# Performance work log

Hardware: AMD Instinct MI355X
Metric: run time of the kernel (lower is better)

Reference implementation:

```python
import jax, jax.numpy as jnp
import numpy as np

DIM, HEADS, DEPTH, SEQ, LOCAL_W = 1024, 16, 7, 2048, 64
HEAD_DIM = DIM // HEADS
SCALE = 1.0 / HEAD_DIM ** 0.5


def cantor_mask(S, depth, local_window):
    """Allowed (i,j): |i-j| within local window, OR |i-j| lies in the Cantor set
    under `depth` levels of ternary subdivision (no base-3 digit equals 1)."""
    idx = np.arange(S)
    d = np.abs(idx[:, None] - idx[None, :])
    x = d.copy()
    ok = np.ones_like(d, dtype=bool)
    for _ in range(depth):
        ok &= (x % 3) != 1
        x //= 3
    ok &= x == 0  # offset must be < 3**depth
    return jnp.asarray(ok | (d <= local_window))  # [S, S] bool


def setup_inputs() -> dict:
    key = jax.random.key(0)
    ks = jax.random.split(key, 8)
    B = 2
    s = 0.02
    return {
        "query": jax.random.normal(ks[0], (B, SEQ, DIM), jnp.float32),
        "key_value": jax.random.normal(ks[1], (B, SEQ, DIM), jnp.float32),
        "Wq": jax.random.normal(ks[2], (DIM, DIM), jnp.float32) * s,
        "bq": jnp.zeros((DIM,), jnp.float32),
        "Wkv": jax.random.normal(ks[3], (DIM, 2 * DIM), jnp.float32) * s,
        "bkv": jnp.zeros((2 * DIM,), jnp.float32),
        "Wo": jax.random.normal(ks[4], (DIM, DIM), jnp.float32) * s,
        "bo": jnp.zeros((DIM,), jnp.float32),
    }


def reference(query, key_value, Wq, bq, Wkv, bkv, Wo, bo):
    B, S, D = query.shape
    H, hd = HEADS, HEAD_DIM
    mask = cantor_mask(S, DEPTH, LOCAL_W)  # static [S, S] bool

    q = (query @ Wq + bq).reshape(B, S, H, hd).transpose(0, 2, 1, 3)  # [B,H,S,hd]
    kv = (key_value @ Wkv + bkv).reshape(B, S, 2, H, hd).transpose(2, 0, 3, 1, 4)
    k, v = kv[0], kv[1]  # [B,H,S,hd]

    scores = jnp.einsum("bhqd,bhkd->bhqk", q, k) * SCALE
    scores = jnp.where(mask, scores, jnp.finfo(scores.dtype).min)
    attn = jax.nn.softmax(scores, axis=-1)
    out = jnp.einsum("bhqk,bhkd->bhqd", attn, v)  # [B,H,S,hd]
    out = out.transpose(0, 2, 1, 3).reshape(B, S, D)
    return out @ Wo + bo
```

## Files before the change

### kernel.cpp

```cpp
#include <hip/hip_runtime.h>
#include <stdint.h>

typedef _Float16 half_t;
typedef __attribute__((ext_vector_type(8))) _Float16 half8;
typedef __attribute__((ext_vector_type(4))) _Float16 half4;
typedef __attribute__((ext_vector_type(4))) float floatx4;

#define SEQ 2048
#define NH 16
#define HD 64

#define MFMA16(a, b, c) __builtin_amdgcn_mfma_f32_16x16x16f16(a, b, c, 0, 0, 0)
#define MFMA32K(a, b, c) __builtin_amdgcn_mfma_f32_16x16x32_f16(a, b, c, 0, 0, 0)

#define QSCALE 0.1803368801111306f

__global__ __launch_bounds__(256) void prep(
    const float* __restrict__ query, const float* __restrict__ key_value,
    const float* __restrict__ Wq, const float* __restrict__ Wkv,
    const float* __restrict__ Wo, half_t* __restrict__ xq,
    half_t* __restrict__ xkv, half_t* __restrict__ wqT,
    half_t* __restrict__ wkvT, half_t* __restrict__ woT,
    uint8_t* __restrict__ tok, uint8_t* __restrict__ tok16,
    uint64_t* __restrict__ maskw) {
  int bx = blockIdx.x, tid = threadIdx.x;
  if (bx < 2048) {
    const float* s; half_t* d; int base;
    if (bx < 1024) { s = query; d = xq; base = bx * 4096; }
    else { s = key_value; d = xkv; base = (bx - 1024) * 4096; }
#pragma unroll
    for (int u = 0; u < 4; ++u) {
      int i = base + u * 1024 + tid * 4;
      floatx4 v = *(const floatx4*)(s + i);
      half4 h;
      h[0] = (half_t)v[0]; h[1] = (half_t)v[1];
      h[2] = (half_t)v[2]; h[3] = (half_t)v[3];
      *(half4*)(d + i) = h;
    }
    return;
  }
  if (bx < 4096) {
    __shared__ float tile[32][33];
    int tx = tid & 31, ty = tid >> 5;
    const int K = 1024;
#pragma unroll
    for (int u = 0; u < 2; ++u) {
      int t = (bx - 2048) * 2 + u;
      const float* W; half_t* Wt; int N, nt, kt;
      if (t < 1024) { W = Wq; Wt = wqT; N = 1024; nt = t & 31; kt = t >> 5; }
      else if (t < 3072) { int t2 = t - 1024; W = Wkv; Wt = wkvT; N = 2048; nt = t2 & 63; kt = t2 >> 6; }
      else { int t2 = t - 3072; W = Wo; Wt = woT; N = 1024; nt = t2 & 31; kt = t2 >> 5; }
      int n0 = nt * 32, k0 = kt * 32;
#pragma unroll
      for (int i = 0; i < 4; ++i)
        tile[ty + i * 8][tx] = W[(size_t)(k0 + ty + i * 8) * N + n0 + tx];
      __syncthreads();
#pragma unroll
      for (int i = 0; i < 4; ++i)
        Wt[(size_t)(n0 + ty + i * 8) * K + k0 + tx] = (half_t)tile[tx][ty + i * 8];
      __syncthreads();
    }
    return;
  }
  __shared__ uint8_t slut[2048];
  int ib = bx - 4096;
  for (int d = tid; d < 2048; d += 256) {
    int x = d;
    bool ok = true;
    for (int it = 0; it < 7; ++it) { ok &= ((x % 3) != 1); x /= 3; }
    ok &= (x == 0);
    slut[d] = (ok || d <= 64) ? 1 : 0;
  }
  __syncthreads();
  if (ib == 0) {
    if (tid < 64) {
      int delta = tid - 32;
      int lo = delta * 64 - 63, hi = delta * 64 + 63;
      uint8_t any = 0;
      for (int x = lo; x <= hi; ++x) {
        int a = x < 0 ? -x : x;
        if (a < 2048) any |= slut[a];
      }
      tok[tid] = any;
    }
    {
      int d16 = tid - 128;
      int ctr = d16 * 16;
      uint8_t any = 0;
      for (int x = ctr - 15; x <= ctr + 15; ++x) {
        int a = x < 0 ? -x : x;
        if (a < 2048) any |= slut[a];
      }
      tok16[tid] = any;
    }
  }
  int g = ib * 256 + tid;
  int tt = g - 2048;
  uint64_t w = 0;
  for (int jj = 0; jj < 64; ++jj) {
    int d = tt - jj; d = d < 0 ? -d : d;
    if (d < 2048 && slut[d]) w |= (1ull << jj);
  }
  maskw[g] = w;
}

__device__ __forceinline__ void cp16(half_t* lds, const half_t* g) {
  __builtin_amdgcn_global_load_lds(
      (const __attribute__((address_space(1))) uint32_t*)g,
      (__attribute__((address_space(3))) uint32_t*)lds, 16, 0, 0);
}

__global__ __launch_bounds__(256) void gemm_qkv(
    const half_t* __restrict__ xq, const half_t* __restrict__ xkv,
    const half_t* __restrict__ wqT, const half_t* __restrict__ wkvT,
    const float* __restrict__ bq, const float* __restrict__ bkv,
    half_t* __restrict__ qout, half_t* __restrict__ kout,
    half_t* __restrict__ vTout) {
  extern __shared__ char smemraw[];
  half_t* As = (half_t*)smemraw;
  half_t* Bs = As + 8192;
  const int K = 1024;
  bool isq = blockIdx.y < 8;
  const half_t* A = isq ? xq : xkv;
  const half_t* Bt = isq ? wqT : wkvT;
  const float* bias = isq ? bq : bkv;
  int n0 = (isq ? blockIdx.y : (blockIdx.y - 8)) * 128;
  int m0 = blockIdx.x * 128;

  int tid = threadIdx.x;
  int wave = tid >> 6, lane = tid & 63;
  int c = lane & 15, quad = lane >> 4;
  int wm = (wave >> 1) * 64, wn = (wave & 1) * 64;

  floatx4 acc[4][4] = {};
  int arow = tid >> 2;
  int akc = ((tid & 3) ^ (arow & 3)) * 8;
  int csw = c & 3;

  cp16(&As[wave * 512], A + (size_t)(m0 + arow) * K + akc);
  cp16(&As[2048 + wave * 512], A + (size_t)(m0 + 64 + arow) * K + akc);
  cp16(&Bs[wave * 512], Bt + (size_t)(n0 + arow) * K + akc);
  cp16(&Bs[2048 + wave * 512], Bt + (size_t)(n0 + 64 + arow) * K + akc);

  for (int kt = 0; kt < 32; ++kt) {
    __syncthreads();
    if (kt + 1 < 32) {
      int k0 = (kt + 1) * 32;
      int b = (kt + 1) & 1;
      cp16(&As[b * 4096 + wave * 512], A + (size_t)(m0 + arow) * K + k0 + akc);
      cp16(&As[b * 4096 + 2048 + wave * 512], A + (size_t)(m0 + 64 + arow) * K + k0 + akc);
      cp16(&Bs[b * 4096 + wave * 512], Bt + (size_t)(n0 + arow) * K + k0 + akc);
      cp16(&Bs[b * 4096 + 2048 + wave * 512], Bt + (size_t)(n0 + 64 + arow) * K + k0 + akc);
    }
    int b = kt & 1;
    half8 af[4], bf[4];
#pragma unroll
    for (int mt = 0; mt < 4; ++mt)
      af[mt] = *(const half8*)&As[b * 4096 + (wm + mt * 16 + c) * 32 + ((quad ^ csw) * 8)];
#pragma unroll
    for (int nt = 0; nt < 4; ++nt)
      bf[nt] = *(const half8*)&Bs[b * 4096 + (wn + nt * 16 + c) * 32 + ((quad ^ csw) * 8)];
#pragma unroll
    for (int mt = 0; mt < 4; ++mt)
#pragma unroll
      for (int nt = 0; nt < 4; ++nt)
        acc[mt][nt] = MFMA32K(af[mt], bf[nt], acc[mt][nt]);
  }

  __syncthreads();
  half_t* ep = (half_t*)smemraw;
  int bb = m0 >> 11, sbase = m0 & 2047;
  bool isv = (!isq) && (n0 >= 1024);

  if (!isv) {
#pragma unroll
    for (int nt = 0; nt < 4; ++nt) {
      int nl = wn + nt * 16 + c;
      float bv = bias[n0 + nl];
#pragma unroll
      for (int mt = 0; mt < 4; ++mt)
#pragma unroll
        for (int r = 0; r < 4; ++r) {
          int ml = wm + mt * 16 + quad * 4 + r;
          float v = acc[mt][nt][r] + bv;
          if (isq) v *= QSCALE;
          ep[ml * 128 + nl] = (half_t)v;
        }
    }
    __syncthreads();
    half_t* outp = isq ? qout : kout;
#pragma unroll
    for (int rd = 0; rd < 8; ++rd) {
      int id = rd * 256 + tid;
      int ml = id >> 4, ch = id & 15;
      int ng = n0 + ch * 8;
      int h = ng >> 6, d0 = ng & 63;
      half8 v = *(const half8*)&ep[ml * 128 + ch * 8];
      *(half8*)(outp + ((size_t)(bb * 16 + h) * SEQ + sbase + ml) * 64 + d0) = v;
    }
  } else {
#pragma unroll
    for (int nt = 0; nt < 4; ++nt) {
      int nl = wn + nt * 16 + c;
      float bv = bias[n0 + nl];
#pragma unroll
      for (int mt = 0; mt < 4; ++mt) {
        int ml = wm + mt * 16 + quad * 4;
        half4 hv;
#pragma unroll
        for (int r = 0; r < 4; ++r) hv[r] = (half_t)(acc[mt][nt][r] + bv);
        *(half4*)&ep[nl * 136 + ml] = hv;
      }
    }
    __syncthreads();
#pragma unroll
    for (int rd = 0; rd < 8; ++rd) {
      int id = rd * 256 + tid;
      int nl = id >> 4, mc = id & 15;
      int ng = n0 + nl;
      int h = (ng >> 6) & 15, d = ng & 63;
      half8 v = *(const half8*)&ep[nl * 136 + mc * 8];
      *(half8*)(vTout + ((size_t)(bb * 16 + h) * 64 + d) * SEQ + sbase + mc * 8) = v;
    }
  }
}

__global__ __launch_bounds__(256) void gemm_out(
    const half_t* __restrict__ A, const half_t* __restrict__ Bt,
    const float* __restrict__ bias, float* __restrict__ outf) {
  __shared__ half_t As[2][128 * 32];
  __shared__ half_t Bs[2][64 * 32];
  const int K = 1024;
  int tid = threadIdx.x;
  int wave = tid >> 6, lane = tid & 63;
  int c = lane & 15, quad = lane >> 4;
  int wm = (wave >> 1) * 64, wn = (wave & 1) * 32;
  int m0 = blockIdx.x * 128, n0 = blockIdx.y * 64;

  floatx4 acc[4][2] = {};
  int arow = tid >> 2;
  int akc = ((tid & 3) ^ (arow & 3)) * 8;
  int csw = c & 3;

  cp16(&As[0][wave * 512], A + (size_t)(m0 + arow) * K + akc);
  cp16(&As[0][2048 + wave * 512], A + (size_t)(m0 + 64 + arow) * K + akc);
  cp16(&Bs[0][wave * 512], Bt + (size_t)(n0 + arow) * K + akc);

  for (int kt = 0; kt < 32; ++kt) {
    __syncthreads();
    if (kt + 1 < 32) {
      int k0 = (kt + 1) * 32;
      int b = (kt + 1) & 1;
      cp16(&As[b][wave * 512], A + (size_t)(m0 + arow) * K + k0 + akc);
      cp16(&As[b][2048 + wave * 512], A + (size_t)(m0 + 64 + arow) * K + k0 + akc);
      cp16(&Bs[b][wave * 512], Bt + (size_t)(n0 + arow) * K + k0 + akc);
    }
    int b = kt & 1;
    half8 af[4], bf[2];
#pragma unroll
    for (int mt = 0; mt < 4; ++mt)
      af[mt] = *(const half8*)&As[b][(wm + mt * 16 + c) * 32 + ((quad ^ csw) * 8)];
#pragma unroll
    for (int nt = 0; nt < 2; ++nt)
      bf[nt] = *(const half8*)&Bs[b][(wn + nt * 16 + c) * 32 + ((quad ^ csw) * 8)];
#pragma unroll
    for (int mt = 0; mt < 4; ++mt)
#pragma unroll
      for (int nt = 0; nt < 2; ++nt)
        acc[mt][nt] = MFMA32K(af[mt], bf[nt], acc[mt][nt]);
  }

#pragma unroll
  for (int nt = 0; nt < 2; ++nt) {
    int n = n0 + wn + nt * 16 + c;
    float bv = bias[n];
#pragma unroll
    for (int mt = 0; mt < 4; ++mt)
#pragma unroll
      for (int r = 0; r < 4; ++r) {
        int m = m0 + wm + mt * 16 + quad * 4 + r;
        outf[(size_t)m * 1024 + n] = acc[mt][nt][r] + bv;
      }
  }
}

__global__ __launch_bounds__(256) void attn_kernel(
    const half_t* __restrict__ qb, const half_t* __restrict__ kb,
    const half_t* __restrict__ vTg, half_t* __restrict__ ctx,
    const uint64_t* __restrict__ maskw, const uint8_t* __restrict__ tok,
    const uint8_t* __restrict__ tok16g) {
  __shared__ half_t kT[64 * 64];
  __shared__ half_t vT[64 * 64];
  __shared__ half_t ot[64 * 72];
  __shared__ int list[34];
  __shared__ uint8_t tok16s[256];
  __shared__ uint32_t mlut[16][2];

  int tid = threadIdx.x, wave = tid >> 6, lane = tid & 63;
  int c = lane & 15, q = lane >> 4;
  int id = blockIdx.x;
  int xcd = id & 7, s = (id >> 3) & 31, bhq = id >> 8;
  int bh = xcd * 4 + bhq;
  int chunk = ((s & 7) << 2) | (s >> 3);
  int i0 = chunk << 6;
  const half_t* qbase = qb + (size_t)bh * SEQ * HD;
  const half_t* kg = kb + (size_t)bh * SEQ * HD;
  const half_t* vg = vTg + (size_t)bh * HD * SEQ;

  tok16s[tid] = tok16g[tid];
  if (tid < 16) {
    mlut[tid][0] = (tid & 1 ? 0xFFFFu : 0u) | (tid & 2 ? 0xFFFF0000u : 0u);
    mlut[tid][1] = (tid & 4 ? 0xFFFFu : 0u) | (tid & 8 ? 0xFFFF0000u : 0u);
  }
  if (wave == 0) {
    int jt = lane;
    bool act = (jt < 32) && tok[(jt - chunk) + 32];
    unsigned long long bal = __ballot(act);
    if (act) {
      int pre = __popcll(bal & ((1ull << jt) - 1));
      list[1 + pre] = jt << 6;
    }
    if (lane == 0) list[0] = __popcll(bal);
  }

  int i_row = i0 + wave * 16 + c;
  int it16 = (i0 >> 4) + wave;
  half8 qf0 = *(const half8*)(qbase + (size_t)i_row * 64 + q * 8);
  half8 qf1 = *(const half8*)(qbase + (size_t)i_row * 64 + 32 + q * 8);

  floatx4 oacc[4] = {};
  floatx4 lacc = {};
  half4 ones;
  ones[0] = (half_t)1.f; ones[1] = (half_t)1.f;
  ones[2] = (half_t)1.f; ones[3] = (half_t)1.f;

  int srow = tid >> 2;
  int sc0 = (tid & 3) * 2;
  int ssw = srow & 7;
  int slotA = (sc0 ^ ssw) * 8;
  int slotB = ((sc0 + 1) ^ ssw) * 8;

  __syncthreads();
  int nact = list[0];
  int j0 = list[1];

  half8 krA = *(const half8*)(kg + (size_t)(j0 + srow) * 64 + sc0 * 8);
  half8 krB = *(const half8*)(kg + (size_t)(j0 + srow) * 64 + sc0 * 8 + 8);
  half8 vrA = *(const half8*)(vg + (size_t)srow * SEQ + j0 + sc0 * 8);
  half8 vrB = *(const half8*)(vg + (size_t)srow * SEQ + j0 + sc0 * 8 + 8);

  for (int ti = 0; ti < nact; ++ti) {
    uint64_t w = maskw[(i_row - j0) + 2048];
    int bidx = (j0 >> 4) - it16 + 128;
    __syncthreads();
    *(half8*)&kT[srow * 64 + slotA] = krA;
    *(half8*)&kT[srow * 64 + slotB] = krB;
    *(half8*)&vT[srow * 64 + slotA] = vrA;
    *(half8*)&vT[srow * 64 + slotB] = vrB;
    int j0n = j0;
    if (ti + 1 < nact) {
      j0n = list[2 + ti];
      krA = *(const half8*)(kg + (size_t)(j0n + srow) * 64 + sc0 * 8);
      krB = *(const half8*)(kg + (size_t)(j0n + srow) * 64 + sc0 * 8 + 8);
      vrA = *(const half8*)(vg + (size_t)srow * SEQ + j0n + sc0 * 8);
      vrB = *(const half8*)(vg + (size_t)srow * SEQ + j0n + sc0 * 8 + 8);
    }
    __syncthreads();

    uint32_t wlo = (uint32_t)(w >> (4 * q));
    uint32_t whi = (uint32_t)(w >> (32 + 4 * q));
#pragma unroll
    for (int jt = 0; jt < 4; ++jt) {
      if (!tok16s[bidx + jt]) continue;
      int row = jt * 16 + c;
      int sw = c & 7;
      half8 a0 = *(const half8*)&kT[row * 64 + ((q ^ sw) * 8)];
      half8 a1 = *(const half8*)&kT[row * 64 + (((4 + q) ^ sw) * 8)];
      floatx4 t = {};
      t = MFMA32K(a0, qf0, t);
      t = MFMA32K(a1, qf1, t);
      uint32_t ww = (jt < 2) ? wlo : whi;
      uint32_t nib = (ww >> (16 * (jt & 1))) & 15u;
      uint32_t m01 = mlut[nib][0];
      uint32_t m23 = mlut[nib][1];
      float p0 = __builtin_exp2f(t[0]);
      float p1 = __builtin_exp2f(t[1]);
      float p2 = __builtin_exp2f(t[2]);
      float p3 = __builtin_exp2f(t[3]);
      auto lo = __builtin_amdgcn_cvt_pkrtz(p0, p1);
      auto hi = __builtin_amdgcn_cvt_pkrtz(p2, p3);
      union { uint32_t u[2]; half4 h4; } pu;
      pu.u[0] = __builtin_bit_cast(uint32_t, lo) & m01;
      pu.u[1] = __builtin_bit_cast(uint32_t, hi) & m23;
      half4 pb = pu.h4;
      lacc = MFMA16(ones, pb, lacc);
#pragma unroll
      for (int mt = 0; mt < 4; ++mt) {
        int drow = mt * 16 + c;
        int ch = 2 * jt + (q >> 1);
        half4 a = *(const half4*)&vT[drow * 64 + ((ch ^ sw) * 8) + (q & 1) * 4];
        oacc[mt] = MFMA16(a, pb, oacc[mt]);
      }
    }
    j0 = j0n;
  }

  float inv_l = 1.0f / lacc[0];
#pragma unroll
  for (int mt = 0; mt < 4; ++mt)
#pragma unroll
    for (int r = 0; r < 4; ++r)
      ot[(wave * 16 + c) * 72 + mt * 16 + 4 * q + r] = (half_t)(oacc[mt][r] * inv_l);
  __syncthreads();
  {
    int row = tid >> 2, chq = tid & 3;
    int b = bh >> 4, h = bh & 15;
    size_t base = (((size_t)(b * SEQ + i0 + row) * NH) + h) * 64 + chq * 16;
    half8 v0 = *(const half8*)&ot[row * 72 + chq * 16];
    half8 v1 = *(const half8*)&ot[row * 72 + chq * 16 + 8];
    *(half8*)(ctx + base) = v0;
    *(half8*)(ctx + base + 8) = v1;
  }
}

extern "C" void kernel_launch(void* const* d_in, const int* in_sizes, int n_in,
                              void* d_out, int out_size, void* d_ws, size_t ws_size,
                              hipStream_t stream) {
  const float* query = (const float*)d_in[0];
  const float* key_value = (const float*)d_in[1];
  const float* Wq = (const float*)d_in[2];
  const float* bq = (const float*)d_in[3];
  const float* Wkv = (const float*)d_in[4];
  const float* bkv = (const float*)d_in[5];
  const float* Wo = (const float*)d_in[6];
  const float* bo = (const float*)d_in[7];

  char* ws = (char*)d_ws;
  uint8_t* tok = (uint8_t*)ws;
  uint8_t* tok16 = (uint8_t*)(ws + 1024);
  uint64_t* maskw = (uint64_t*)(ws + 4096);
  const size_t MB = 1ull << 20;
  half_t* xq = (half_t*)(ws + 1 * MB);
  half_t* xkv = (half_t*)(ws + 9 * MB);
  half_t* wqT = (half_t*)(ws + 17 * MB);
  half_t* wkvT = (half_t*)(ws + 19 * MB);
  half_t* woT = (half_t*)(ws + 23 * MB);
  half_t* qbuf = (half_t*)(ws + 25 * MB);
  half_t* kbuf = (half_t*)(ws + 33 * MB);
  half_t* vTg = (half_t*)(ws + 41 * MB);
  half_t* ctx = xq;

  hipLaunchKernelGGL(prep, dim3(4112), dim3(256), 0, stream,
                     query, key_value, Wq, Wkv, Wo, xq, xkv, wqT, wkvT, woT,
                     tok, tok16, maskw);
  hipLaunchKernelGGL(gemm_qkv, dim3(32, 24), dim3(256), 34816, stream,
                     xq, xkv, wqT, wkvT, bq, bkv, qbuf, kbuf, vTg);
  hipLaunchKernelGGL(attn_kernel, dim3(1024), dim3(256), 0, stream,
                     qbuf, kbuf, vTg, ctx, maskw, tok, tok16);
  hipLaunchKernelGGL(gemm_out, dim3(32, 16), dim3(256), 0, stream,
                     ctx, woT, bo, (float*)d_out);
}
```

Baseline: 224.3 us.

## Read K/V fragments directly from global memory instead of LDS staging in attention

```diff
diff --git a/kernel.cpp b/kernel.cpp
--- a/kernel.cpp
+++ b/kernel.cpp
@@ -284,43 +284,44 @@
   }
 }
 
-__global__ __launch_bounds__(256) void attn_kernel(
+__global__ __launch_bounds__(512) void attn_kernel(
     const half_t* __restrict__ qb, const half_t* __restrict__ kb,
     const half_t* __restrict__ vTg, half_t* __restrict__ ctx,
     const uint64_t* __restrict__ maskw, const uint8_t* __restrict__ tok,
     const uint8_t* __restrict__ tok16g) {
-  __shared__ half_t kT[64 * 64];
-  __shared__ half_t vT[64 * 64];
-  __shared__ half_t ot[64 * 72];
-  __shared__ int list[34];
+  __shared__ half_t ot[128 * 72];
+  __shared__ int listA[33];
+  __shared__ int listB[33];
   __shared__ uint8_t tok16s[256];
   __shared__ uint32_t mlut[16][2];
 
   int tid = threadIdx.x, wave = tid >> 6, lane = tid & 63;
   int c = lane & 15, q = lane >> 4;
   int id = blockIdx.x;
-  int xcd = id & 7, s = (id >> 3) & 31, bhq = id >> 8;
-  int bh = xcd * 4 + bhq;
-  int chunk = ((s & 7) << 2) | (s >> 3);
-  int i0 = chunk << 6;
+  int bh = (id & 7) * 4 + ((id >> 3) & 3);
+  int it128 = id >> 5;
+  int i0 = it128 << 7;
   const half_t* qbase = qb + (size_t)bh * SEQ * HD;
   const half_t* kg = kb + (size_t)bh * SEQ * HD;
   const half_t* vg = vTg + (size_t)bh * HD * SEQ;
 
-  tok16s[tid] = tok16g[tid];
-  if (tid < 16) {
-    mlut[tid][0] = (tid & 1 ? 0xFFFFu : 0u) | (tid & 2 ? 0xFFFF0000u : 0u);
-    mlut[tid][1] = (tid & 4 ? 0xFFFFu : 0u) | (tid & 8 ? 0xFFFF0000u : 0u);
-  }
-  if (wave == 0) {
+  if (tid < 256) tok16s[tid] = tok16g[tid];
+  if (tid >= 256 && tid < 272) {
+    int t = tid - 256;
+    mlut[t][0] = (t & 1 ? 0xFFFFu : 0u) | (t & 2 ? 0xFFFF0000u : 0u);
+    mlut[t][1] = (t & 4 ? 0xFFFFu : 0u) | (t & 8 ? 0xFFFF0000u : 0u);
+  }
+  if (wave < 2) {
     int jt = lane;
-    bool act = (jt < 32) && tok[(jt - chunk) + 32];
+    int chunkw = (i0 >> 6) + wave;
+    bool act = (jt < 32) && tok[(jt - chunkw) + 32];
     unsigned long long bal = __ballot(act);
+    int* L = wave ? listB : listA;
     if (act) {
       int pre = __popcll(bal & ((1ull << jt) - 1));
-      list[1 + pre] = jt << 6;
-    }
-    if (lane == 0) list[0] = __popcll(bal);
+      L[1 + pre] = jt << 6;
+    }
+    if (lane == 0) L[0] = __popcll(bal);
   }
 
   int i_row = i0 + wave * 16 + c;
@@ -334,48 +335,23 @@
   ones[0] = (half_t)1.f; ones[1] = (half_t)1.f;
   ones[2] = (half_t)1.f; ones[3] = (half_t)1.f;
 
-  int srow = tid >> 2;
-  int sc0 = (tid & 3) * 2;
-  int ssw = srow & 7;
-  int slotA = (sc0 ^ ssw) * 8;
-  int slotB = ((sc0 + 1) ^ ssw) * 8;
-
   __syncthreads();
-  int nact = list[0];
-  int j0 = list[1];
-
-  half8 krA = *(const half8*)(kg + (size_t)(j0 + srow) * 64 + sc0 * 8);
-  half8 krB = *(const half8*)(kg + (size_t)(j0 + srow) * 64 + sc0 * 8 + 8);
-  half8 vrA = *(const half8*)(vg + (size_t)srow * SEQ + j0 + sc0 * 8);
-  half8 vrB = *(const half8*)(vg + (size_t)srow * SEQ + j0 + sc0 * 8 + 8);
+  const int* myl = (wave >= 4) ? listB : listA;
+  int nact = myl[0];
 
   for (int ti = 0; ti < nact; ++ti) {
+    int j0 = myl[1 + ti];
     uint64_t w = maskw[(i_row - j0) + 2048];
     int bidx = (j0 >> 4) - it16 + 128;
-    __syncthreads();
-    *(half8*)&kT[srow * 64 + slotA] = krA;
-    *(half8*)&kT[srow * 64 + slotB] = krB;
-    *(half8*)&vT[srow * 64 + slotA] = vrA;
-    *(half8*)&vT[srow * 64 + slotB] = vrB;
-    int j0n = j0;
-    if (ti + 1 < nact) {
-      j0n = list[2 + ti];
-      krA = *(const half8*)(kg + (size_t)(j0n + srow) * 64 + sc0 * 8);
-      krB = *(const half8*)(kg + (size_t)(j0n + srow) * 64 + sc0 * 8 + 8);
-      vrA = *(const half8*)(vg + (size_t)srow * SEQ + j0n + sc0 * 8);
-      vrB = *(const half8*)(vg + (size_t)srow * SEQ + j0n + sc0 * 8 + 8);
-    }
-    __syncthreads();
-
     uint32_t wlo = (uint32_t)(w >> (4 * q));
     uint32_t whi = (uint32_t)(w >> (32 + 4 * q));
+    const half_t* kb0 = kg + (size_t)(j0 + c) * 64 + q * 8;
+    const half_t* vb0 = vg + (size_t)c * SEQ + j0 + 4 * q;
 #pragma unroll
     for (int jt = 0; jt < 4; ++jt) {
       if (!tok16s[bidx + jt]) continue;
-      int row = jt * 16 + c;
-      int sw = c & 7;
-      half8 a0 = *(const half8*)&kT[row * 64 + ((q ^ sw) * 8)];
-      half8 a1 = *(const half8*)&kT[row * 64 + (((4 + q) ^ sw) * 8)];
+      half8 a0 = *(const half8*)(kb0 + jt * 1024);
+      half8 a1 = *(const half8*)(kb0 + jt * 1024 + 32);
       floatx4 t = {};
       t = MFMA32K(a0, qf0, t);
       t = MFMA32K(a1, qf1, t);
@@ -396,13 +372,10 @@
       lacc = MFMA16(ones, pb, lacc);
 #pragma unroll
       for (int mt = 0; mt < 4; ++mt) {
-        int drow = mt * 16 + c;
-        int ch = 2 * jt + (q >> 1);
-        half4 a = *(const half4*)&vT[drow * 64 + ((ch ^ sw) * 8) + (q & 1) * 4];
+        half4 a = *(const half4*)(vb0 + (size_t)mt * 16 * SEQ + jt * 16);
         oacc[mt] = MFMA16(a, pb, oacc[mt]);
       }
     }
-    j0 = j0n;
   }
 
   float inv_l = 1.0f / lacc[0];
@@ -455,7 +428,7 @@
                      tok, tok16, maskw);
   hipLaunchKernelGGL(gemm_qkv, dim3(32, 24), dim3(256), 34816, stream,
                      xq, xkv, wqT, wkvT, bq, bkv, qbuf, kbuf, vTg);
-  hipLaunchKernelGGL(attn_kernel, dim3(1024), dim3(256), 0, stream,
+  hipLaunchKernelGGL(attn_kernel, dim3(512), dim3(512), 0, stream,
                      qbuf, kbuf, vTg, ctx, maskw, tok, tok16);
   hipLaunchKernelGGL(gemm_out, dim3(32, 16), dim3(256), 0, stream,
                      ctx, woT, bo, (float*)d_out);
```

After: 313.6 us. +39.8%, slower.
